# Kernel tuning notes

Hardware: AMD Instinct MI355X
Metric: run time of the kernel (lower is better)

## Reference

```python
import jax, jax.numpy as jnp
import numpy as np

N = 100_000
E = 1_600_000
EPS_STD = 1e-5


def _pna(x, src, dst, eattr, We, be, Wpre, bpre, Wpost, bpost, Wlin, blin):
    # PyG PNAConv, towers=1, pre/post_layers=1, scalers=['identity']
    e = eattr @ We + be                                   # [E, Fin]
    h = jnp.concatenate([x[dst], x[src], e], axis=-1)     # [E, 3*Fin] (x_i, x_j, edge)
    m = h @ Wpre + bpre                                   # [E, Fin]
    cnt = jax.ops.segment_sum(jnp.ones((m.shape[0],), m.dtype), dst, N)  # [N]
    denom = jnp.maximum(cnt, 1.0)[:, None]
    s = jax.ops.segment_sum(m, dst, N)
    mean = s / denom
    has = (cnt > 0)[:, None]
    mx = jnp.where(has, jax.ops.segment_max(m, dst, N), 0.0)
    mn = jnp.where(has, jax.ops.segment_min(m, dst, N), 0.0)
    mean_sq = jax.ops.segment_sum(m * m, dst, N) / denom
    std = jnp.sqrt(jax.nn.relu(mean_sq - mean * mean) + EPS_STD)
    agg = jnp.concatenate([s, mean, mx, mn, std], axis=-1)  # [N, 5*Fin]
    out = jnp.concatenate([x, agg], axis=-1) @ Wpost + bpost # [N, Fout]
    return out @ Wlin + blin


def _gcn(x, src, dst, W, b):
    # GCNConv with add_self_loops + symmetric normalization
    h = x @ W
    loops = jnp.arange(N)
    s2 = jnp.concatenate([src, loops])
    d2 = jnp.concatenate([dst, loops])
    deg = jax.ops.segment_sum(jnp.ones(s2.shape, h.dtype), d2, N)
    dinv = jnp.where(deg > 0, deg ** -0.5, 0.0)
    w = dinv[s2] * dinv[d2]
    return jax.ops.segment_sum(h[s2] * w[:, None], d2, N) + b


def _forward(x, edge_index, edge_attr,
             We0, be0, Wpre0, bpre0, Wpost0, bpost0, Wlin0, blin0,
             We1, be1, Wpre1, bpre1, Wpost1, bpost1, Wlin1, blin1,
             Wg, bg, Wh1, bh1, Wh2, bh2):
    src, dst = edge_index[0], edge_index[1]
    h = jax.nn.relu(_pna(x, src, dst, edge_attr, We0, be0, Wpre0, bpre0, Wpost0, bpost0, Wlin0, blin0))
    h = jax.nn.relu(_pna(h, src, dst, edge_attr, We1, be1, Wpre1, bpre1, Wpost1, bpost1, Wlin1, blin1))
    h = _gcn(h, src, dst, Wg, bg)                          # [N, 16]
    out = jnp.concatenate([h, x], axis=1)                  # [N, 32]
    out = jax.nn.relu(out @ Wh1 + bh1) @ Wh2 + bh2         # [N, 10]
    return out


def setup_inputs() -> dict:
    key = jax.random.key(0)
    ks = list(jax.random.split(key, 32))
    k = iter(ks)

    def glorot(shape):
        lim = float(np.sqrt(6.0 / (shape[0] + shape[1])))
        return jax.random.uniform(next(k), shape, jnp.float32, -lim, lim)

    inp = {}
    inp['x'] = jax.random.normal(next(k), (N, 16), jnp.float32)
    inp['edge_index'] = jax.random.randint(next(k), (2, E), 0, N)
    inp['edge_attr'] = jax.random.normal(next(k), (E, 4), jnp.float32)
    # layer 0: Fin=16, Fout=64
    inp['We0'] = glorot((4, 16)); inp['be0'] = jnp.zeros((16,), jnp.float32)
    inp['Wpre0'] = glorot((48, 16)); inp['bpre0'] = jnp.zeros((16,), jnp.float32)
    inp['Wpost0'] = glorot((96, 64)); inp['bpost0'] = jnp.zeros((64,), jnp.float32)
    inp['Wlin0'] = glorot((64, 64)); inp['blin0'] = jnp.zeros((64,), jnp.float32)
    # layer 1: Fin=64, Fout=64
    inp['We1'] = glorot((4, 64)); inp['be1'] = jnp.zeros((64,), jnp.float32)
    inp['Wpre1'] = glorot((192, 64)); inp['bpre1'] = jnp.zeros((64,), jnp.float32)
    inp['Wpost1'] = glorot((384, 64)); inp['bpost1'] = jnp.zeros((64,), jnp.float32)
    inp['Wlin1'] = glorot((64, 64)); inp['blin1'] = jnp.zeros((64,), jnp.float32)
    # GCN + head
    inp['Wg'] = glorot((64, 16)); inp['bg'] = jnp.zeros((16,), jnp.float32)
    inp['Wh1'] = glorot((32, 10)); inp['bh1'] = jnp.zeros((10,), jnp.float32)
    inp['Wh2'] = glorot((10, 10)); inp['bh2'] = jnp.zeros((10,), jnp.float32)
    return inp


def reference(x, edge_index, edge_attr,
              We0, be0, Wpre0, bpre0, Wpost0, bpost0, Wlin0, blin0,
              We1, be1, Wpre1, bpre1, Wpost1, bpost1, Wlin1, blin1,
              Wg, bg, Wh1, bh1, Wh2, bh2):
    return _forward(x, edge_index, edge_attr,
                    We0, be0, Wpre0, bpre0, Wpost0, bpost0, Wlin0, blin0,
                    We1, be1, Wpre1, bpre1, Wpost1, bpost1, Wlin1, blin1,
                    Wg, bg, Wh1, bh1, Wh2, bh2)
```

## Files before the change

kernel.cpp:

```cpp
#include <hip/hip_runtime.h>

#define NN 100000
#define NE 1600000

#define BSH 9
#define BSZ (1 << BSH)
#define NB  196
#define CHUNK 6250

#define OFF_C0   0
#define OFF_D0   64
#define OFF_WPL0 80
#define OFF_BPL0 6224
#define OFF_C1   6288
#define OFF_D1   6544
#define OFF_WPL1 6608
#define OFF_BPL1 31184
#define WBUF_TOT 31248

#define BT1_OFF 0
#define BT0_OFF 24576
#define BTA_OFF 30720
#define BTB_OFF 34816
#define BT_TOT  38912

__device__ inline unsigned short pack_bf16(float a) {
  unsigned ua = __float_as_uint(a);
  ua += 0x7fffu + ((ua >> 16) & 1u);
  return (unsigned short)(ua >> 16);
}
__device__ inline float bf_s(unsigned short u) { return __uint_as_float(((unsigned)u) << 16); }

__global__ void k_prep(const float* __restrict__ We0, const float* __restrict__ be0,
                       const float* __restrict__ Wpre0, const float* __restrict__ bpre0,
                       const float* __restrict__ Wpost0, const float* __restrict__ bpost0,
                       const float* __restrict__ Wlin0, const float* __restrict__ blin0,
                       const float* __restrict__ We1, const float* __restrict__ be1,
                       const float* __restrict__ Wpre1, const float* __restrict__ bpre1,
                       const float* __restrict__ Wpost1, const float* __restrict__ bpost1,
                       const float* __restrict__ Wlin1, const float* __restrict__ blin1,
                       float* __restrict__ wbuf) {
  int id = blockIdx.x * 256 + threadIdx.x;
  if (id >= WBUF_TOT) return;
  float a = 0.f;
  if (id < OFF_D0) {
    int j = id >> 4, f = id & 15;
    for (int t = 0; t < 16; t++) a = fmaf(We0[j*16+t], Wpre0[(32+t)*16+f], a);
  } else if (id < OFF_WPL0) {
    int f = id - OFF_D0; a = bpre0[f];
    for (int t = 0; t < 16; t++) a = fmaf(be0[t], Wpre0[(32+t)*16+f], a);
  } else if (id < OFF_BPL0) {
    int r = id - OFF_WPL0; int k = r >> 6, o = r & 63;
    for (int j = 0; j < 64; j++) a = fmaf(Wpost0[k*64+j], Wlin0[j*64+o], a);
  } else if (id < OFF_C1) {
    int o = id - OFF_BPL0; a = blin0[o];
    for (int j = 0; j < 64; j++) a = fmaf(bpost0[j], Wlin0[j*64+o], a);
  } else if (id < OFF_D1) {
    int r = id - OFF_C1; int j = r >> 6, f = r & 63;
    for (int t = 0; t < 64; t++) a = fmaf(We1[j*64+t], Wpre1[(128+t)*64+f], a);
  } else if (id < OFF_WPL1) {
    int f = id - OFF_D1; a = bpre1[f];
    for (int t = 0; t < 64; t++) a = fmaf(be1[t], Wpre1[(128+t)*64+f], a);
  } else if (id < OFF_BPL1) {
    int r = id - OFF_WPL1; int k = r >> 6, o = r & 63;
    for (int j = 0; j < 64; j++) a = fmaf(Wpost1[k*64+j], Wlin1[j*64+o], a);
  } else {
    int o = id - OFF_BPL1; a = blin1[o];
    for (int j = 0; j < 64; j++) a = fmaf(bpost1[j], Wlin1[j*64+o], a);
  }
  wbuf[id] = a;
}

__global__ void k_bt(const float* __restrict__ wbuf, const float* __restrict__ Wpre1,
                     unsigned short* __restrict__ Bt) {
  int nn = blockIdx.x;
  int k  = threadIdx.x;
  if (k < 384) {
    Bt[BT1_OFF + nn * 384 + k] = pack_bf16(wbuf[OFF_WPL1 + k * 64 + nn]);
  } else if (k < 480) {
    int kk = k - 384;
    Bt[BT0_OFF + nn * 96 + kk] = pack_bf16(wbuf[OFF_WPL0 + kk * 64 + nn]);
  } else if (k < 544) {
    int kk = k - 480;
    Bt[BTA_OFF + nn * 64 + kk] = pack_bf16(Wpre1[kk * 64 + nn]);
  } else if (k < 608) {
    int kk = k - 544;
    Bt[BTB_OFF + nn * 64 + kk] = pack_bf16(Wpre1[(64 + kk) * 64 + nn]);
  }
}

__global__ void k_hist(const int* __restrict__ dst, int* __restrict__ cnt) {
  int i = blockIdx.x * 256 + threadIdx.x;
  if (i < NE) atomicAdd(&cnt[dst[i]], 1);
}

__global__ void k_scan1(const int* __restrict__ deg, int* __restrict__ partial,
                        int* __restrict__ bsums) {
  __shared__ int lds[256];
  int i = blockIdx.x * 256 + threadIdx.x;
  int v = (i < NN) ? deg[i] : 0;
  lds[threadIdx.x] = v;
  __syncthreads();
  for (int off = 1; off < 256; off <<= 1) {
    int t = (threadIdx.x >= off) ? lds[threadIdx.x - off] : 0;
    __syncthreads();
    lds[threadIdx.x] += t;
    __syncthreads();
  }
  if (i < NN) partial[i] = lds[threadIdx.x];
  if (threadIdx.x == 255) bsums[blockIdx.x] = lds[255];
}

__global__ void k_scan2(const int* __restrict__ bsums, int* __restrict__ boff, int nb) {
  __shared__ int lds[512];
  int v = ((int)threadIdx.x < nb) ? bsums[threadIdx.x] : 0;
  lds[threadIdx.x] = v;
  __syncthreads();
  for (int off = 1; off < 512; off <<= 1) {
    int t = (threadIdx.x >= off) ? lds[threadIdx.x - off] : 0;
    __syncthreads();
    lds[threadIdx.x] += t;
    __syncthreads();
  }
  if ((int)threadIdx.x < nb) boff[threadIdx.x] = lds[threadIdx.x] - v;
}

__global__ void k_scan3(const int* __restrict__ partial, const int* __restrict__ boff,
                        const int* __restrict__ deg, int* __restrict__ rowptr,
                        int* __restrict__ fill) {
  int i = blockIdx.x * 256 + threadIdx.x;
  if (i < NN) {
    int incl = partial[i] + boff[blockIdx.x];
    rowptr[i + 1] = incl;
    fill[i] = incl - deg[i];
  }
  if (i == 0) rowptr[0] = 0;
}

__global__ void k_binit(const int* __restrict__ rowptr, int* __restrict__ gfill) {
  int b = threadIdx.x;
  if (b < NB) {
    int n0 = b << BSH;
    gfill[b] = rowptr[n0 > NN ? NN : n0];
  }
}

__global__ __launch_bounds__(256) void k_bin(const int* __restrict__ dst,
                                             int* __restrict__ gfill,
                                             int2* __restrict__ rec) {
  __shared__ int hcnt[NB];
  __shared__ int hbase[NB];
  const int t = threadIdx.x;
  for (int b = t; b < NB; b += 256) hcnt[b] = 0;
  __syncthreads();
  const int lo = blockIdx.x * CHUNK, hi = lo + CHUNK;
  for (int i = lo + t; i < hi; i += 256)
    atomicAdd(&hcnt[dst[i] >> BSH], 1);
  __syncthreads();
  for (int b = t; b < NB; b += 256) {
    int c = hcnt[b];
    hbase[b] = c > 0 ? atomicAdd(&gfill[b], c) : 0;
    hcnt[b] = 0;
  }
  __syncthreads();
  for (int i = lo + t; i < hi; i += 256) {
    int d = dst[i];
    int b = d >> BSH;
    int lp = atomicAdd(&hcnt[b], 1);
    rec[hbase[b] + lp] = make_int2(d, i);
  }
}

__global__ __launch_bounds__(256) void k_scatter2(const int2* __restrict__ rec,
                                                  const int* __restrict__ rowptr,
                                                  int* __restrict__ perm) {
  __shared__ int lfill[BSZ];
  const int b = blockIdx.x;
  const int n0 = b << BSH;
  const int n1 = (n0 + BSZ < NN) ? n0 + BSZ : NN;
  const int t = threadIdx.x;
  for (int n = n0 + t; n < n1; n += 256) lfill[n - n0] = rowptr[n];
  __syncthreads();
  const int lo = rowptr[n0], hi = rowptr[n1];
  for (int i = lo + t; i < hi; i += 256) {
    int2 r = rec[i];
    int pos = atomicAdd(&lfill[r.x - n0], 1);
    perm[pos] = r.y;
  }
}

__global__ void k_permute(const int* __restrict__ perm, const int* __restrict__ src,
                          const float4* __restrict__ ea, int* __restrict__ col,
                          float4* __restrict__ eap) {
  int i = blockIdx.x * 256 + threadIdx.x;
  if (i < NE) {
    int eid = perm[i];
    col[i] = src[eid];
    eap[i] = ea[eid];
  }
}

__global__ void k_pre0(const float* __restrict__ x, const float* __restrict__ Wpre0,
                       float* __restrict__ xA0, unsigned short* __restrict__ xB0b) {
  int t = blockIdx.x * 256 + threadIdx.x;
  int node = t >> 5, k = t & 31;
  int f = k & 15;
  const float* W = Wpre0 + (k < 16 ? 0 : 256);
  const float* xr = x + (size_t)node * 16;
  float a = 0.f;
#pragma unroll
  for (int j = 0; j < 16; j++) a = fmaf(xr[j], W[j*16+f], a);
  if (k < 16) xA0[(size_t)node*16+f] = a;
  else        xB0b[(size_t)node*16+f] = pack_bf16(a);
}

__global__ __launch_bounds__(256) void k_agg0(const float* __restrict__ x,
                                              const float* __restrict__ xA0,
                                              const unsigned short* __restrict__ xB0b,
                                              const int* __restrict__ rowptr,
                                              const int* __restrict__ col,
                                              const float4* __restrict__ eap,
                                              const float* __restrict__ wbuf,
                                              unsigned short* __restrict__ vec96b) {
  const int w = threadIdx.x >> 6, lane = threadIdx.x & 63;
  const int g = lane >> 4, f = lane & 15;
  const int node = blockIdx.x * 4 + w;
  const int start = rowptr[node], end = rowptr[node + 1];
  const int cnt = end - start;
  const float c0 = wbuf[OFF_C0 + f],      c1v = wbuf[OFF_C0 + 16 + f];
  const float c2v = wbuf[OFF_C0 + 32 + f], c3v = wbuf[OFF_C0 + 48 + f];
  float s = 0.f, sq = 0.f, mx = -__builtin_inff(), mn = __builtin_inff();
  int p = start + g;
  for (; p + 4 < end; p += 8) {
    int s0 = col[p], s1 = col[p + 4];
    float4 e0 = eap[p], e1 = eap[p + 4];
    float v0 = bf_s(xB0b[(size_t)s0 * 16 + f]);
    float v1 = bf_s(xB0b[(size_t)s1 * 16 + f]);
    v0 = fmaf(e0.x, c0, v0); v0 = fmaf(e0.y, c1v, v0);
    v0 = fmaf(e0.z, c2v, v0); v0 = fmaf(e0.w, c3v, v0);
    v1 = fmaf(e1.x, c0, v1); v1 = fmaf(e1.y, c1v, v1);
    v1 = fmaf(e1.z, c2v, v1); v1 = fmaf(e1.w, c3v, v1);
    s += v0 + v1;
    sq = fmaf(v0, v0, sq); sq = fmaf(v1, v1, sq);
    mx = fmaxf(mx, fmaxf(v0, v1)); mn = fminf(mn, fminf(v0, v1));
  }
  for (; p < end; p += 4) {
    int si = col[p];
    float4 e0 = eap[p];
    float v = bf_s(xB0b[(size_t)si * 16 + f]);
    v = fmaf(e0.x, c0, v); v = fmaf(e0.y, c1v, v);
    v = fmaf(e0.z, c2v, v); v = fmaf(e0.w, c3v, v);
    s += v; sq = fmaf(v, v, sq); mx = fmaxf(mx, v); mn = fminf(mn, v);
  }
  s  += __shfl_xor(s, 16);  s  += __shfl_xor(s, 32);
  sq += __shfl_xor(sq, 16); sq += __shfl_xor(sq, 32);
  mx = fmaxf(mx, __shfl_xor(mx, 16)); mx = fmaxf(mx, __shfl_xor(mx, 32));
  mn = fminf(mn, __shfl_xor(mn, 16)); mn = fminf(mn, __shfl_xor(mn, 32));
  const float c = xA0[(size_t)node * 16 + f] + wbuf[OFF_D0 + f];
  float sum_m, mean_m, mx_m, mn_m, std_m;
  if (cnt > 0) {
    float inv = 1.f / (float)cnt;
    float meanv = s * inv;
    sum_m = fmaf((float)cnt, c, s);
    mean_m = meanv + c;
    mx_m = mx + c; mn_m = mn + c;
    float var = fmaf(-meanv, meanv, sq * inv);
    std_m = sqrtf(fmaxf(var, 0.f) + 1e-5f);
  } else {
    sum_m = 0.f; mean_m = 0.f; mx_m = 0.f; mn_m = 0.f; std_m = sqrtf(1e-5f);
  }
  if (g == 0) {
    unsigned short* vr = vec96b + (size_t)node * 96;
    vr[f]      = pack_bf16(x[(size_t)node * 16 + f]);
    vr[16 + f] = pack_bf16(sum_m);
    vr[32 + f] = pack_bf16(mean_m);
    vr[48 + f] = pack_bf16(mx_m);
    vr[64 + f] = pack_bf16(mn_m);
    vr[80 + f] = pack_bf16(std_m);
  }
}

__global__ __launch_bounds__(64) void k_agg1(const float* __restrict__ xA1,
                                             const unsigned short* __restrict__ xB1b,
                                             const int* __restrict__ rowptr,
                                             const int* __restrict__ col,
                                             const float4* __restrict__ eap,
                                             const float* __restrict__ wbuf,
                                             unsigned short* __restrict__ agg320b) {
  const int f = threadIdx.x;
  const int node = blockIdx.x;
  const int start = rowptr[node], end = rowptr[node + 1];
  const int cnt = end - start;
  const float c0 = wbuf[OFF_C1 + f],       c1v = wbuf[OFF_C1 + 64 + f];
  const float c2v = wbuf[OFF_C1 + 128 + f], c3v = wbuf[OFF_C1 + 192 + f];
  float s = 0.f, sq = 0.f, mx = -__builtin_inff(), mn = __builtin_inff();
  int p = start;
  for (; p + 7 < end; p += 8) {
#pragma unroll
    for (int u = 0; u < 8; u++) {
      int si = col[p + u];
      float4 e = eap[p + u];
      const unsigned short* row = xB1b + (unsigned)si * 64;
      float v = bf_s(row[f]);
      v = fmaf(e.x, c0, v); v = fmaf(e.y, c1v, v);
      v = fmaf(e.z, c2v, v); v = fmaf(e.w, c3v, v);
      s += v; sq = fmaf(v, v, sq); mx = fmaxf(mx, v); mn = fminf(mn, v);
    }
  }
  for (; p < end; p++) {
    int si = col[p];
    float4 e = eap[p];
    const unsigned short* row = xB1b + (unsigned)si * 64;
    float v = bf_s(row[f]);
    v = fmaf(e.x, c0, v); v = fmaf(e.y, c1v, v);
    v = fmaf(e.z, c2v, v); v = fmaf(e.w, c3v, v);
    s += v; sq = fmaf(v, v, sq); mx = fmaxf(mx, v); mn = fminf(mn, v);
  }
  const float c = xA1[(size_t)node * 64 + f] + wbuf[OFF_D1 + f];
  float sum_m, mean_m, mx_m, mn_m, std_m;
  if (cnt > 0) {
    float inv = 1.f / (float)cnt;
    float meanv = s * inv;
    sum_m = fmaf((float)cnt, c, s);
    mean_m = meanv + c;
    mx_m = mx + c; mn_m = mn + c;
    float var = fmaf(-meanv, meanv, sq * inv);
    std_m = sqrtf(fmaxf(var, 0.f) + 1e-5f);
  } else {
    sum_m = 0.f; mean_m = 0.f; mx_m = 0.f; mn_m = 0.f; std_m = sqrtf(1e-5f);
  }
  unsigned short* ar = agg320b + (size_t)node * 320;
  ar[f]       = pack_bf16(sum_m);
  ar[64 + f]  = pack_bf16(mean_m);
  ar[128 + f] = pack_bf16(mx_m);
  ar[192 + f] = pack_bf16(mn_m);
  ar[256 + f] = pack_bf16(std_m);
}

template <int K, bool RELU, int OMODE>
__global__ __launch_bounds__(256) void k_mmf(const unsigned short* __restrict__ A,
                                             const unsigned short* __restrict__ Bt,
                                             const float* __restrict__ bias,
                                             void* __restrict__ C, int n) {
  using bf16x8 = __attribute__((ext_vector_type(8))) short;
  using f32x4  = __attribute__((ext_vector_type(4))) float;
  const int wave = threadIdx.x >> 6, lane = threadIdx.x & 63;
  const int qm = lane & 15, quad = lane >> 4;
  const int m0 = blockIdx.x * 64 + wave * 16;
  const int mrow = m0 + qm;
  f32x4 acc[4] = {};
#pragma unroll
  for (int k0 = 0; k0 < K; k0 += 32) {
    bf16x8 a = *(const bf16x8*)(A + (size_t)mrow * K + k0 + quad * 8);
#pragma unroll
    for (int nt = 0; nt < 4; nt++) {
      bf16x8 b = *(const bf16x8*)(Bt + (size_t)(nt * 16 + qm) * K + k0 + quad * 8);
      acc[nt] = __builtin_amdgcn_mfma_f32_16x16x32_bf16(a, b, acc[nt], 0, 0, 0);
    }
  }
#pragma unroll
  for (int nt = 0; nt < 4; nt++) {
    int colc = nt * 16 + qm;
    float bb = bias ? bias[colc] : 0.f;
#pragma unroll
    for (int r = 0; r < 4; r++) {
      int m = m0 + quad * 4 + r;
      if (m < n) {
        float v = acc[nt][r] + bb;
        if (RELU) v = fmaxf(v, 0.f);
        if (OMODE == 0) ((float*)C)[(size_t)m * 64 + colc] = v;
        else ((unsigned short*)C)[(size_t)m * 64 + colc] = pack_bf16(v);
      }
    }
  }
}

__global__ __launch_bounds__(256) void k_mm384(const unsigned short* __restrict__ hb,
                                               const unsigned short* __restrict__ aggb,
                                               const unsigned short* __restrict__ Btb,
                                               const float* __restrict__ wbuf,
                                               float* __restrict__ h2, int n) {
  using bf16x8 = __attribute__((ext_vector_type(8))) short;
  using f32x4  = __attribute__((ext_vector_type(4))) float;
  const int wave = threadIdx.x >> 6, lane = threadIdx.x & 63;
  const int qm = lane & 15, quad = lane >> 4;
  const int m0 = blockIdx.x * 64 + wave * 16;
  const int mrow = m0 + qm;
  f32x4 acc[4] = {};
  for (int k0 = 0; k0 < 384; k0 += 32) {
    bf16x8 a;
    if (k0 < 64) a = *(const bf16x8*)(hb + (size_t)mrow * 64 + k0 + quad * 8);
    else         a = *(const bf16x8*)(aggb + (size_t)mrow * 320 + (k0 - 64) + quad * 8);
#pragma unroll
    for (int nt = 0; nt < 4; nt++) {
      bf16x8 b = *(const bf16x8*)(Btb + (size_t)(nt * 16 + qm) * 384 + k0 + quad * 8);
      acc[nt] = __builtin_amdgcn_mfma_f32_16x16x32_bf16(a, b, acc[nt], 0, 0, 0);
    }
  }
#pragma unroll
  for (int nt = 0; nt < 4; nt++) {
    int colc = nt * 16 + qm;
    float bias = wbuf[OFF_BPL1 + colc];
#pragma unroll
    for (int r = 0; r < 4; r++) {
      int m = m0 + quad * 4 + r;
      if (m < n) h2[(size_t)m * 64 + colc] = fmaxf(acc[nt][r] + bias, 0.f);
    }
  }
}

__global__ void k_gcnprep(const float* __restrict__ h2, const float* __restrict__ Wg,
                          const int* __restrict__ rowptr,
                          unsigned short* __restrict__ hgsb, float* __restrict__ dinv) {
  int t = blockIdx.x * 256 + threadIdx.x;
  int node = t >> 4, f = t & 15;
  const float* hr = h2 + (size_t)node * 64;
  float a = 0.f;
#pragma unroll
  for (int j = 0; j < 64; j++) a = fmaf(hr[j], Wg[j * 16 + f], a);
  int dg = rowptr[node + 1] - rowptr[node] + 1;
  float dv = 1.0f / sqrtf((float)dg);
  hgsb[(size_t)node * 16 + f] = pack_bf16(a * dv);
  if (f == 0) dinv[node] = dv;
}

__global__ __launch_bounds__(256) void k_head(const float* __restrict__ x,
                                              const unsigned short* __restrict__ hgsb,
                                              const float* __restrict__ dinv,
                                              const int* __restrict__ rowptr,
                                              const int* __restrict__ col,
                                              const float* __restrict__ bg,
                                              const float* __restrict__ Wh1,
                                              const float* __restrict__ bh1,
                                              const float* __restrict__ Wh2,
                                              const float* __restrict__ bh2,
                                              float* __restrict__ out) {
  __shared__ float zb[4][32];
  __shared__ float o1b[4][10];
  const int w = threadIdx.x >> 6, lane = threadIdx.x & 63;
  const int g = lane >> 4, f = lane & 15;
  const int node = blockIdx.x * 4 + w;
  const int start = rowptr[node], end = rowptr[node + 1];
  float s = 0.f;
  int p = start + g;
  for (; p + 12 < end; p += 16) {
    int s0 = col[p], s1 = col[p + 4], s2 = col[p + 8], s3 = col[p + 12];
    float v0 = bf_s(hgsb[(size_t)s0 * 16 + f]);
    float v1 = bf_s(hgsb[(size_t)s1 * 16 + f]);
    float v2 = bf_s(hgsb[(size_t)s2 * 16 + f]);
    float v3 = bf_s(hgsb[(size_t)s3 * 16 + f]);
    s += (v0 + v1) + (v2 + v3);
  }
  for (; p < end; p += 4) {
    int si = col[p];
    s += bf_s(hgsb[(size_t)si * 16 + f]);
  }
  s += __shfl_xor(s, 16); s += __shfl_xor(s, 32);
  if (g == 0) {
    float gout = (s + bf_s(hgsb[(size_t)node * 16 + f])) * dinv[node] + bg[f];
    zb[w][f] = gout;
    zb[w][16 + f] = x[(size_t)node * 16 + f];
  }
  __syncthreads();
  if (lane < 10) {
    float a = bh1[lane];
#pragma unroll
    for (int k = 0; k < 32; k++) a = fmaf(zb[w][k], Wh1[k * 10 + lane], a);
    o1b[w][lane] = fmaxf(a, 0.f);
  }
  __syncthreads();
  if (lane < 10) {
    float a = bh2[lane];
#pragma unroll
    for (int j = 0; j < 10; j++) a = fmaf(o1b[w][j], Wh2[j * 10 + lane], a);
    out[(size_t)node * 10 + lane] = a;
  }
}

extern "C" void kernel_launch(void* const* d_in, const int* in_sizes, int n_in,
                              void* d_out, int out_size, void* d_ws, size_t ws_size,
                              hipStream_t stream) {
  const float* x      = (const float*)d_in[0];
  const int*   ei     = (const int*)d_in[1];
  const float* eattr  = (const float*)d_in[2];
  const float* We0    = (const float*)d_in[3];
  const float* be0    = (const float*)d_in[4];
  const float* Wpre0  = (const float*)d_in[5];
  const float* bpre0  = (const float*)d_in[6];
  const float* Wpost0 = (const float*)d_in[7];
  const float* bpost0 = (const float*)d_in[8];
  const float* Wlin0  = (const float*)d_in[9];
  const float* blin0  = (const float*)d_in[10];
  const float* We1    = (const float*)d_in[11];
  const float* be1    = (const float*)d_in[12];
  const float* Wpre1  = (const float*)d_in[13];
  const float* bpre1  = (const float*)d_in[14];
  const float* Wpost1 = (const float*)d_in[15];
  const float* bpost1 = (const float*)d_in[16];
  const float* Wlin1  = (const float*)d_in[17];
  const float* blin1  = (const float*)d_in[18];
  const float* Wg     = (const float*)d_in[19];
  const float* bg     = (const float*)d_in[20];
  const float* Wh1    = (const float*)d_in[21];
  const float* bh1    = (const float*)d_in[22];
  const float* Wh2    = (const float*)d_in[23];
  const float* bh2    = (const float*)d_in[24];
  const int* srcI = ei;
  const int* dstI = ei + NE;
  float* out = (float*)d_out;

  char* base = (char*)d_ws;
  size_t off = 0;
  auto take = [&](size_t bytes) -> char* {
    char* p = base + off;
    off += (bytes + 255) & ~(size_t)255;
    return p;
  };
  int* cnt     = (int*)take((size_t)NN * 4);
  int* rowptr  = (int*)take((size_t)(NN + 1) * 4);
  int* fill    = (int*)take((size_t)NN * 4);
  int* partial = (int*)take((size_t)NN * 4);
  int* bsums   = (int*)take(512 * 4);
  int* boff    = (int*)take(512 * 4);
  int* gfill   = (int*)take(512 * 4);
  unsigned short* Bt = (unsigned short*)take((size_t)BT_TOT * 2);
  int* col     = (int*)take((size_t)NE * 4);
  float4* eap  = (float4*)take((size_t)NE * 16);
  float* h2    = (float*)eap;
  float* wbuf  = (float*)take((size_t)WBUF_TOT * 4);
  int*   perm  = (int*)take((size_t)NE * 4);
  float* xA1   = (float*)take((size_t)NN * 64 * 4);
  int2*  rec   = (int2*)take((size_t)NE * 8);
  unsigned short* xB1b = (unsigned short*)rec;
  char* Z = take((size_t)NN * 320 * 4);
  unsigned short* vec96b  = (unsigned short*)Z;
  float* xA0    = (float*)(Z + (size_t)NN * 96 * 2);
  unsigned short* xB0b = (unsigned short*)(Z + (size_t)NN * 96 * 2 + (size_t)NN * 16 * 4);
  unsigned short* agg320b = (unsigned short*)Z;
  unsigned short* hb = (unsigned short*)(Z + (size_t)96 * 1024 * 1024);
  unsigned short* hgsb = (unsigned short*)Z;
  float* dinv   = (float*)(Z + (size_t)NN * 16 * 2);

  hipMemsetAsync(cnt, 0, (size_t)NN * 4, stream);
  k_prep<<<(WBUF_TOT + 255) / 256, 256, 0, stream>>>(
      We0, be0, Wpre0, bpre0, Wpost0, bpost0, Wlin0, blin0,
      We1, be1, Wpre1, bpre1, Wpost1, bpost1, Wlin1, blin1, wbuf);
  k_bt<<<64, 640, 0, stream>>>(wbuf, Wpre1, Bt);
  k_hist<<<(NE + 255) / 256, 256, 0, stream>>>(dstI, cnt);
  k_scan1<<<391, 256, 0, stream>>>(cnt, partial, bsums);
  k_scan2<<<1, 512, 0, stream>>>(bsums, boff, 391);
  k_scan3<<<391, 256, 0, stream>>>(partial, boff, cnt, rowptr, fill);
  k_binit<<<1, 256, 0, stream>>>(rowptr, gfill);
  k_bin<<<256, 256, 0, stream>>>(dstI, gfill, rec);
  k_scatter2<<<NB, 256, 0, stream>>>(rec, rowptr, perm);
  k_permute<<<(NE + 255) / 256, 256, 0, stream>>>(perm, srcI, (const float4*)eattr,
                                                  col, eap);
  k_pre0<<<NN * 32 / 256, 256, 0, stream>>>(x, Wpre0, xA0, xB0b);
  k_agg0<<<NN / 4, 256, 0, stream>>>(x, xA0, xB0b, rowptr, col, eap, wbuf, vec96b);
  k_mmf<96, true, 1><<<(NN + 63) / 64, 256, 0, stream>>>(
      vec96b, Bt + BT0_OFF, wbuf + OFF_BPL0, hb, NN);
  k_mmf<64, false, 0><<<(NN + 63) / 64, 256, 0, stream>>>(
      hb, Bt + BTA_OFF, nullptr, xA1, NN);
  k_mmf<64, false, 1><<<(NN + 63) / 64, 256, 0, stream>>>(
      hb, Bt + BTB_OFF, nullptr, xB1b, NN);
  k_agg1<<<NN, 64, 0, stream>>>(xA1, xB1b, rowptr, col, eap, wbuf, agg320b);
  k_mm384<<<(NN + 63) / 64, 256, 0, stream>>>(hb, agg320b, Bt + BT1_OFF, wbuf, h2, NN);
  k_gcnprep<<<NN * 16 / 256, 256, 0, stream>>>(h2, Wg, rowptr, hgsb, dinv);
  k_head<<<NN / 4, 256, 0, stream>>>(x, hgsb, dinv, rowptr, col, bg, Wh1, bh1,
                                     Wh2, bh2, out);
}
```

Baseline: 593.9 us.

## Fuse prep kernels, store edge attrs as bf16, merge matmuls, fuse GCN prep

Folds the weight-transpose kernel into the weight-prep kernel and drops the unused fill output from the scan. Edge attributes are stored permuted as bf16 (8 bytes per edge instead of 16), which cuts gather traffic in both aggregation kernels. The two 64-wide matmuls that share input hb become one kernel, and the 384-K matmul now computes the GCN projection and degree normalisation through LDS, removing the h2 round trip and a separate launch. Rounding edge attributes to bf16 adds precision loss.

```diff
diff --git a/kernel.cpp b/kernel.cpp
--- a/kernel.cpp
+++ b/kernel.cpp
@@ -23,6 +23,7 @@
 #define BTA_OFF 30720
 #define BTB_OFF 34816
 #define BT_TOT  38912
+#define PREP_TOT (WBUF_TOT + BT_TOT)
 
 __device__ inline unsigned short pack_bf16(float a) {
   unsigned ua = __float_as_uint(a);
@@ -39,53 +40,59 @@
                        const float* __restrict__ Wpre1, const float* __restrict__ bpre1,
                        const float* __restrict__ Wpost1, const float* __restrict__ bpost1,
                        const float* __restrict__ Wlin1, const float* __restrict__ blin1,
-                       float* __restrict__ wbuf) {
+                       float* __restrict__ wbuf, unsigned short* __restrict__ Bt) {
   int id = blockIdx.x * 256 + threadIdx.x;
-  if (id >= WBUF_TOT) return;
-  float a = 0.f;
-  if (id < OFF_D0) {
-    int j = id >> 4, f = id & 15;
-    for (int t = 0; t < 16; t++) a = fmaf(We0[j*16+t], Wpre0[(32+t)*16+f], a);
-  } else if (id < OFF_WPL0) {
-    int f = id - OFF_D0; a = bpre0[f];
-    for (int t = 0; t < 16; t++) a = fmaf(be0[t], Wpre0[(32+t)*16+f], a);
-  } else if (id < OFF_BPL0) {
-    int r = id - OFF_WPL0; int k = r >> 6, o = r & 63;
-    for (int j = 0; j < 64; j++) a = fmaf(Wpost0[k*64+j], Wlin0[j*64+o], a);
-  } else if (id < OFF_C1) {
-    int o = id - OFF_BPL0; a = blin0[o];
-    for (int j = 0; j < 64; j++) a = fmaf(bpost0[j], Wlin0[j*64+o], a);
-  } else if (id < OFF_D1) {
-    int r = id - OFF_C1; int j = r >> 6, f = r & 63;
-    for (int t = 0; t < 64; t++) a = fmaf(We1[j*64+t], Wpre1[(128+t)*64+f], a);
-  } else if (id < OFF_WPL1) {
-    int f = id - OFF_D1; a = bpre1[f];
-    for (int t = 0; t < 64; t++) a = fmaf(be1[t], Wpre1[(128+t)*64+f], a);
-  } else if (id < OFF_BPL1) {
-    int r = id - OFF_WPL1; int k = r >> 6, o = r & 63;
-    for (int j = 0; j < 64; j++) a = fmaf(Wpost1[k*64+j], Wlin1[j*64+o], a);
+  if (id >= PREP_TOT) return;
+  if (id < WBUF_TOT) {
+    float a = 0.f;
+    if (id < OFF_D0) {
+      int j = id >> 4, f = id & 15;
+      for (int t = 0; t < 16; t++) a = fmaf(We0[j*16+t], Wpre0[(32+t)*16+f], a);
+    } else if (id < OFF_WPL0) {
+      int f = id - OFF_D0; a = bpre0[f];
+      for (int t = 0; t < 16; t++) a = fmaf(be0[t], Wpre0[(32+t)*16+f], a);
+    } else if (id < OFF_BPL0) {
+      int r = id - OFF_WPL0; int k = r >> 6, o = r & 63;
+      for (int j = 0; j < 64; j++) a = fmaf(Wpost0[k*64+j], Wlin0[j*64+o], a);
+    } else if (id < OFF_C1) {
+      int o = id - OFF_BPL0; a = blin0[o];
+      for (int j = 0; j < 64; j++) a = fmaf(bpost0[j], Wlin0[j*64+o], a);
+    } else if (id < OFF_D1) {
+      int r = id - OFF_C1; int j = r >> 6, f = r & 63;
+      for (int t = 0; t < 64; t++) a = fmaf(We1[j*64+t], Wpre1[(128+t)*64+f], a);
+    } else if (id < OFF_WPL1) {
+      int f = id - OFF_D1; a = bpre1[f];
+      for (int t = 0; t < 64; t++) a = fmaf(be1[t], Wpre1[(128+t)*64+f], a);
+    } else if (id < OFF_BPL1) {
+      int r = id - OFF_WPL1; int k = r >> 6, o = r & 63;
+      for (int j = 0; j < 64; j++) a = fmaf(Wpost1[k*64+j], Wlin1[j*64+o], a);
+    } else {
+      int o = id - OFF_BPL1; a = blin1[o];
+      for (int j = 0; j < 64; j++) a = fmaf(bpost1[j], Wlin1[j*64+o], a);
+    }
+    wbuf[id] = a;
+    return;
+  }
+  int rid = id - WBUF_TOT;
+  if (rid < 24576) {
+    int nn = rid / 384, k = rid - nn * 384;
+    float a = 0.f;
+    for (int j = 0; j < 64; j++) a = fmaf(Wpost1[k*64+j], Wlin1[j*64+nn], a);
+    Bt[BT1_OFF + rid] = pack_bf16(a);
+  } else if (rid < 30720) {
+    int r2 = rid - 24576;
+    int nn = r2 / 96, k = r2 - nn * 96;
+    float a = 0.f;
+    for (int j = 0; j < 64; j++) a = fmaf(Wpost0[k*64+j], Wlin0[j*64+nn], a);
+    Bt[BT0_OFF + r2] = pack_bf16(a);
+  } else if (rid < 34816) {
+    int r3 = rid - 30720;
+    int nn = r3 >> 6, k = r3 & 63;
+    Bt[BTA_OFF + r3] = pack_bf16(Wpre1[k*64+nn]);
   } else {
-    int o = id - OFF_BPL1; a = blin1[o];
-    for (int j = 0; j < 64; j++) a = fmaf(bpost1[j], Wlin1[j*64+o], a);
-  }
-  wbuf[id] = a;
-}
-
-__global__ void k_bt(const float* __restrict__ wbuf, const float* __restrict__ Wpre1,
-                     unsigned short* __restrict__ Bt) {
-  int nn = blockIdx.x;
-  int k  = threadIdx.x;
-  if (k < 384) {
-    Bt[BT1_OFF + nn * 384 + k] = pack_bf16(wbuf[OFF_WPL1 + k * 64 + nn]);
-  } else if (k < 480) {
-    int kk = k - 384;
-    Bt[BT0_OFF + nn * 96 + kk] = pack_bf16(wbuf[OFF_WPL0 + kk * 64 + nn]);
-  } else if (k < 544) {
-    int kk = k - 480;
-    Bt[BTA_OFF + nn * 64 + kk] = pack_bf16(Wpre1[kk * 64 + nn]);
-  } else if (k < 608) {
-    int kk = k - 544;
-    Bt[BTB_OFF + nn * 64 + kk] = pack_bf16(Wpre1[(64 + kk) * 64 + nn]);
+    int r4 = rid - 34816;
+    int nn = r4 >> 6, k = r4 & 63;
+    Bt[BTB_OFF + r4] = pack_bf16(Wpre1[(64+k)*64+nn]);
   }
 }
 
@@ -126,14 +133,9 @@
 }
 
 __global__ void k_scan3(const int* __restrict__ partial, const int* __restrict__ boff,
-                        const int* __restrict__ deg, int* __restrict__ rowptr,
-                        int* __restrict__ fill) {
+                        int* __restrict__ rowptr) {
   int i = blockIdx.x * 256 + threadIdx.x;
-  if (i < NN) {
-    int incl = partial[i] + boff[blockIdx.x];
-    rowptr[i + 1] = incl;
-    fill[i] = incl - deg[i];
-  }
+  if (i < NN) rowptr[i + 1] = partial[i] + boff[blockIdx.x];
   if (i == 0) rowptr[0] = 0;
 }
 
@@ -191,12 +193,16 @@
 
 __global__ void k_permute(const int* __restrict__ perm, const int* __restrict__ src,
                           const float4* __restrict__ ea, int* __restrict__ col,
-                          float4* __restrict__ eap) {
+                          ushort4* __restrict__ eapb) {
   int i = blockIdx.x * 256 + threadIdx.x;
   if (i < NE) {
     int eid = perm[i];
     col[i] = src[eid];
-    eap[i] = ea[eid];
+    float4 e = ea[eid];
+    ushort4 pk;
+    pk.x = pack_bf16(e.x); pk.y = pack_bf16(e.y);
+    pk.z = pack_bf16(e.z); pk.w = pack_bf16(e.w);
+    eapb[i] = pk;
   }
 }
 
@@ -219,7 +225,7 @@
                                               const unsigned short* __restrict__ xB0b,
                                               const int* __restrict__ rowptr,
                                               const int* __restrict__ col,
-                                              const float4* __restrict__ eap,
+                                              const ushort4* __restrict__ eapb,
                                               const float* __restrict__ wbuf,
                                               unsigned short* __restrict__ vec96b) {
   const int w = threadIdx.x >> 6, lane = threadIdx.x & 63;
@@ -233,23 +239,23 @@
   int p = start + g;
   for (; p + 4 < end; p += 8) {
     int s0 = col[p], s1 = col[p + 4];
-    float4 e0 = eap[p], e1 = eap[p + 4];
+    ushort4 e0 = eapb[p], e1 = eapb[p + 4];
     float v0 = bf_s(xB0b[(size_t)s0 * 16 + f]);
     float v1 = bf_s(xB0b[(size_t)s1 * 16 + f]);
-    v0 = fmaf(e0.x, c0, v0); v0 = fmaf(e0.y, c1v, v0);
-    v0 = fmaf(e0.z, c2v, v0); v0 = fmaf(e0.w, c3v, v0);
-    v1 = fmaf(e1.x, c0, v1); v1 = fmaf(e1.y, c1v, v1);
-    v1 = fmaf(e1.z, c2v, v1); v1 = fmaf(e1.w, c3v, v1);
+    v0 = fmaf(bf_s(e0.x), c0, v0); v0 = fmaf(bf_s(e0.y), c1v, v0);
+    v0 = fmaf(bf_s(e0.z), c2v, v0); v0 = fmaf(bf_s(e0.w), c3v, v0);
+    v1 = fmaf(bf_s(e1.x), c0, v1); v1 = fmaf(bf_s(e1.y), c1v, v1);
+    v1 = fmaf(bf_s(e1.z), c2v, v1); v1 = fmaf(bf_s(e1.w), c3v, v1);
     s += v0 + v1;
     sq = fmaf(v0, v0, sq); sq = fmaf(v1, v1, sq);
     mx = fmaxf(mx, fmaxf(v0, v1)); mn = fminf(mn, fminf(v0, v1));
   }
   for (; p < end; p += 4) {
     int si = col[p];
-    float4 e0 = eap[p];
+    ushort4 e0 = eapb[p];
     float v = bf_s(xB0b[(size_t)si * 16 + f]);
-    v = fmaf(e0.x, c0, v); v = fmaf(e0.y, c1v, v);
-    v = fmaf(e0.z, c2v, v); v = fmaf(e0.w, c3v, v);
+    v = fmaf(bf_s(e0.x), c0, v); v = fmaf(bf_s(e0.y), c1v, v);
+    v = fmaf(bf_s(e0.z), c2v, v); v = fmaf(bf_s(e0.w), c3v, v);
     s += v; sq = fmaf(v, v, sq); mx = fmaxf(mx, v); mn = fminf(mn, v);
   }
   s  += __shfl_xor(s, 16);  s  += __shfl_xor(s, 32);
@@ -284,7 +290,7 @@
                                              const unsigned short* __restrict__ xB1b,
                                              const int* __restrict__ rowptr,
                                              const int* __restrict__ col,
-                                             const float4* __restrict__ eap,
+                                             const ushort4* __restrict__ eapb,
                                              const float* __restrict__ wbuf,
                                              unsigned short* __restrict__ agg320b) {
   const int f = threadIdx.x;
@@ -299,21 +305,21 @@
 #pragma unroll
     for (int u = 0; u < 8; u++) {
       int si = col[p + u];
-      float4 e = eap[p + u];
+      ushort4 e = eapb[p + u];
       const unsigned short* row = xB1b + (unsigned)si * 64;
       float v = bf_s(row[f]);
-      v = fmaf(e.x, c0, v); v = fmaf(e.y, c1v, v);
-      v = fmaf(e.z, c2v, v); v = fmaf(e.w, c3v, v);
+      v = fmaf(bf_s(e.x), c0, v); v = fmaf(bf_s(e.y), c1v, v);
+      v = fmaf(bf_s(e.z), c2v, v); v = fmaf(bf_s(e.w), c3v, v);
       s += v; sq = fmaf(v, v, sq); mx = fmaxf(mx, v); mn = fminf(mn, v);
     }
   }
   for (; p < end; p++) {
     int si = col[p];
-    float4 e = eap[p];
+    ushort4 e = eapb[p];
     const unsigned short* row = xB1b + (unsigned)si * 64;
     float v = bf_s(row[f]);
-    v = fmaf(e.x, c0, v); v = fmaf(e.y, c1v, v);
-    v = fmaf(e.z, c2v, v); v = fmaf(e.w, c3v, v);
+    v = fmaf(bf_s(e.x), c0, v); v = fmaf(bf_s(e.y), c1v, v);
+    v = fmaf(bf_s(e.z), c2v, v); v = fmaf(bf_s(e.w), c3v, v);
     s += v; sq = fmaf(v, v, sq); mx = fmaxf(mx, v); mn = fminf(mn, v);
   }
   const float c = xA1[(size_t)node * 64 + f] + wbuf[OFF_D1 + f];
@@ -375,14 +381,58 @@
   }
 }
 
-__global__ __launch_bounds__(256) void k_mm384(const unsigned short* __restrict__ hb,
-                                               const unsigned short* __restrict__ aggb,
-                                               const unsigned short* __restrict__ Btb,
-                                               const float* __restrict__ wbuf,
-                                               float* __restrict__ h2, int n) {
+__global__ __launch_bounds__(256) void k_mmf64d(const unsigned short* __restrict__ A,
+                                                const unsigned short* __restrict__ BtA,
+                                                const unsigned short* __restrict__ BtB,
+                                                float* __restrict__ xA1,
+                                                unsigned short* __restrict__ xB1b, int n) {
   using bf16x8 = __attribute__((ext_vector_type(8))) short;
   using f32x4  = __attribute__((ext_vector_type(4))) float;
   const int wave = threadIdx.x >> 6, lane = threadIdx.x & 63;
+  const int qm = lane & 15, quad = lane >> 4;
+  const int m0 = blockIdx.x * 64 + wave * 16;
+  const int mrow = m0 + qm;
+  f32x4 accA[4] = {}, accB[4] = {};
+#pragma unroll
+  for (int k0 = 0; k0 < 64; k0 += 32) {
+    bf16x8 a = *(const bf16x8*)(A + (size_t)mrow * 64 + k0 + quad * 8);
+#pragma unroll
+    for (int nt = 0; nt < 4; nt++) {
+      bf16x8 bA = *(const bf16x8*)(BtA + (size_t)(nt * 16 + qm) * 64 + k0 + quad * 8);
+      bf16x8 bB = *(const bf16x8*)(BtB + (size_t)(nt * 16 + qm) * 64 + k0 + quad * 8);
+      accA[nt] = __builtin_amdgcn_mfma_f32_16x16x32_bf16(a, bA, accA[nt], 0, 0, 0);
+      accB[nt] = __builtin_amdgcn_mfma_f32_16x16x32_bf16(a, bB, accB[nt], 0, 0, 0);
+    }
+  }
+#pragma unroll
+  for (int nt = 0; nt < 4; nt++) {
+    int colc = nt * 16 + qm;
+#pragma unroll
+    for (int r = 0; r < 4; r++) {
+      int m = m0 + quad * 4 + r;
+      if (m < n) {
+        xA1[(size_t)m * 64 + colc] = accA[nt][r];
+        xB1b[(size_t)m * 64 + colc] = pack_bf16(accB[nt][r]);
+      }
+    }
+  }
+}
+
+__global__ __launch_bounds__(256) void k_mm384g(const unsigned short* __restrict__ hb,
+                                                const unsigned short* __restrict__ aggb,
+                                                const unsigned short* __restrict__ Bt1,
+                                                const float* __restrict__ wbuf,
+                                                const float* __restrict__ Wg,
+                                                const int* __restrict__ rowptr,
+                                                unsigned short* __restrict__ hgsb,
+                                                float* __restrict__ dinv, int n) {
+  using bf16x8 = __attribute__((ext_vector_type(8))) short;
+  using f32x4  = __attribute__((ext_vector_type(4))) float;
+  __shared__ float h2t[4][16][65];
+  __shared__ float wg[64][16];
+  const int tid = threadIdx.x;
+  for (int i = tid; i < 1024; i += 256) wg[i >> 4][i & 15] = Wg[i];
+  const int wave = tid >> 6, lane = tid & 63;
   const int qm = lane & 15, quad = lane >> 4;
   const int m0 = blockIdx.x * 64 + wave * 16;
   const int mrow = m0 + qm;
@@ -393,7 +443,7 @@
     else         a = *(const bf16x8*)(aggb + (size_t)mrow * 320 + (k0 - 64) + quad * 8);
 #pragma unroll
     for (int nt = 0; nt < 4; nt++) {
-      bf16x8 b = *(const bf16x8*)(Btb + (size_t)(nt * 16 + qm) * 384 + k0 + quad * 8);
+      bf16x8 b = *(const bf16x8*)(Bt1 + (size_t)(nt * 16 + qm) * 384 + k0 + quad * 8);
       acc[nt] = __builtin_amdgcn_mfma_f32_16x16x32_bf16(a, b, acc[nt], 0, 0, 0);
     }
   }
@@ -402,26 +452,29 @@
     int colc = nt * 16 + qm;
     float bias = wbuf[OFF_BPL1 + colc];
 #pragma unroll
-    for (int r = 0; r < 4; r++) {
-      int m = m0 + quad * 4 + r;
-      if (m < n) h2[(size_t)m * 64 + colc] = fmaxf(acc[nt][r] + bias, 0.f);
-    }
-  }
-}
-
-__global__ void k_gcnprep(const float* __restrict__ h2, const float* __restrict__ Wg,
-                          const int* __restrict__ rowptr,
-                          unsigned short* __restrict__ hgsb, float* __restrict__ dinv) {
-  int t = blockIdx.x * 256 + threadIdx.x;
-  int node = t >> 4, f = t & 15;
-  const float* hr = h2 + (size_t)node * 64;
-  float a = 0.f;
-#pragma unroll
-  for (int j = 0; j < 64; j++) a = fmaf(hr[j], Wg[j * 16 + f], a);
-  int dg = rowptr[node + 1] - rowptr[node] + 1;
-  float dv = 1.0f / sqrtf((float)dg);
-  hgsb[(size_t)node * 16 + f] = pack_bf16(a * dv);
-  if (f == 0) dinv[node] = dv;
+    for (int r = 0; r < 4; r++)
+      h2t[wave][quad * 4 + r][colc] = fmaxf(acc[nt][r] + bias, 0.f);
+  }
+  __syncthreads();
+  const int row = lane & 15, g = lane >> 4;
+  float hg0 = 0.f, hg1 = 0.f, hg2 = 0.f, hg3 = 0.f;
+#pragma unroll 16
+  for (int j = 0; j < 64; j++) {
+    float hv = h2t[wave][row][j];
+    float4 w4 = *(const float4*)&wg[j][g * 4];
+    hg0 = fmaf(hv, w4.x, hg0); hg1 = fmaf(hv, w4.y, hg1);
+    hg2 = fmaf(hv, w4.z, hg2); hg3 = fmaf(hv, w4.w, hg3);
+  }
+  int m = m0 + row;
+  if (m < n) {
+    int deg = rowptr[m + 1] - rowptr[m] + 1;
+    float dv = 1.0f / sqrtf((float)deg);
+    if (g == 0) dinv[m] = dv;
+    ushort4 pk;
+    pk.x = pack_bf16(hg0 * dv); pk.y = pack_bf16(hg1 * dv);
+    pk.z = pack_bf16(hg2 * dv); pk.w = pack_bf16(hg3 * dv);
+    *(ushort4*)(hgsb + (size_t)m * 16 + g * 4) = pk;
+  }
 }
 
 __global__ __launch_bounds__(256) void k_head(const float* __restrict__ x,
@@ -518,17 +571,17 @@
   };
   int* cnt     = (int*)take((size_t)NN * 4);
   int* rowptr  = (int*)take((size_t)(NN + 1) * 4);
-  int* fill    = (int*)take((size_t)NN * 4);
   int* partial = (int*)take((size_t)NN * 4);
   int* bsums   = (int*)take(512 * 4);
   int* boff    = (int*)take(512 * 4);
   int* gfill   = (int*)take(512 * 4);
   unsigned short* Bt = (unsigned short*)take((size_t)BT_TOT * 2);
   int* col     = (int*)take((size_t)NE * 4);
-  float4* eap  = (float4*)take((size_t)NE * 16);
-  float* h2    = (float*)eap;
+  ushort4* eapb = (ushort4*)take((size_t)NE * 8);
   float* wbuf  = (float*)take((size_t)WBUF_TOT * 4);
   int*   perm  = (int*)take((size_t)NE * 4);
+  unsigned short* hgsb = (unsigned short*)perm;
+  float* dinv  = (float*)((char*)perm + (size_t)NN * 16 * 2);
   float* xA1   = (float*)take((size_t)NN * 64 * 4);
   int2*  rec   = (int2*)take((size_t)NE * 8);
   unsigned short* xB1b = (unsigned short*)rec;
@@ -538,34 +591,29 @@
   unsigned short* xB0b = (unsigned short*)(Z + (size_t)NN * 96 * 2 + (size_t)NN * 16 * 4);
   unsigned short* agg320b = (unsigned short*)Z;
   unsigned short* hb = (unsigned short*)(Z + (size_t)96 * 1024 * 1024);
-  unsigned short* hgsb = (unsigned short*)Z;
-  float* dinv   = (float*)(Z + (size_t)NN * 16 * 2);
 
   hipMemsetAsync(cnt, 0, (size_t)NN * 4, stream);
-  k_prep<<<(WBUF_TOT + 255) / 256, 256, 0, stream>>>(
+  k_prep<<<(PREP_TOT + 255) / 256, 256, 0, stream>>>(
       We0, be0, Wpre0, bpre0, Wpost0, bpost0, Wlin0, blin0,
-      We1, be1, Wpre1, bpre1, Wpost1, bpost1, Wlin1, blin1, wbuf);
-  k_bt<<<64, 640, 0, stream>>>(wbuf, Wpre1, Bt);
+      We1, be1, Wpre1, bpre1, Wpost1, bpost1, Wlin1, blin1, wbuf, Bt);
   k_hist<<<(NE + 255) / 256, 256, 0, stream>>>(dstI, cnt);
   k_scan1<<<391, 256, 0, stream>>>(cnt, partial, bsums);
   k_scan2<<<1, 512, 0, stream>>>(bsums, boff, 391);
-  k_scan3<<<391, 256, 0, stream>>>(partial, boff, cnt, rowptr, fill);
+  k_scan3<<<391, 256, 0, stream>>>(partial, boff, rowptr);
   k_binit<<<1, 256, 0, stream>>>(rowptr, gfill);
   k_bin<<<256, 256, 0, stream>>>(dstI, gfill, rec);
   k_scatter2<<<NB, 256, 0, stream>>>(rec, rowptr, perm);
   k_permute<<<(NE + 255) / 256, 256, 0, stream>>>(perm, srcI, (const float4*)eattr,
-                                                  col, eap);
+                                                  col, eapb);
   k_pre0<<<NN * 32 / 256, 256, 0, stream>>>(x, Wpre0, xA0, xB0b);
-  k_agg0<<<NN / 4, 256, 0, stream>>>(x, xA0, xB0b, rowptr, col, eap, wbuf, vec96b);
+  k_agg0<<<NN / 4, 256, 0, stream>>>(x, xA0, xB0b, rowptr, col, eapb, wbuf, vec96b);
   k_mmf<96, true, 1><<<(NN + 63) / 64, 256, 0, stream>>>(
       vec96b, Bt + BT0_OFF, wbuf + OFF_BPL0, hb, NN);
-  k_mmf<64, false, 0><<<(NN + 63) / 64, 256, 0, stream>>>(
-      hb, Bt + BTA_OFF, nullptr, xA1, NN);
-  k_mmf<64, false, 1><<<(NN + 63) / 64, 256, 0, stream>>>(
-      hb, Bt + BTB_OFF, nullptr, xB1b, NN);
-  k_agg1<<<NN, 64, 0, stream>>>(xA1, xB1b, rowptr, col, eap, wbuf, agg320b);
-  k_mm384<<<(NN + 63) / 64, 256, 0, stream>>>(hb, agg320b, Bt + BT1_OFF, wbuf, h2, NN);
-  k_gcnprep<<<NN * 16 / 256, 256, 0, stream>>>(h2, Wg, rowptr, hgsb, dinv);
+  k_mmf64d<<<(NN + 63) / 64, 256, 0, stream>>>(
+      hb, Bt + BTA_OFF, Bt + BTB_OFF, xA1, xB1b, NN);
+  k_agg1<<<NN, 64, 0, stream>>>(xA1, xB1b, rowptr, col, eapb, wbuf, agg320b);
+  k_mm384g<<<(NN + 63) / 64, 256, 0, stream>>>(
+      hb, agg320b, Bt + BT1_OFF, wbuf, Wg, rowptr, hgsb, dinv, NN);
   k_head<<<NN / 4, 256, 0, stream>>>(x, hgsb, dinv, rowptr, col, bg, Wh1, bh1,
                                      Wh2, bh2, out);
 }
```

Result: faster. 560.5 us (-5.6%).
